# Performance work log

Measured on AMD Instinct MI355X. Metric: run time of the kernel, lower is better.

The kernel has to match this reference:

```python
import jax, jax.numpy as jnp
import numpy as np

BLOCK_SIZE = 32
EPS = 1e-6


def setup_inputs() -> dict:
    key = jax.random.key(0)
    k1, k2, k3, k4, k5 = jax.random.split(key, 5)
    B, H, L, D = 2, 16, 4096, 128
    return {
        "query_states": jax.random.normal(k1, (B, H, L, D), dtype=jnp.float32),
        "key_states": jax.random.normal(k2, (B, H, L, D), dtype=jnp.float32),
        "value_states": jax.random.normal(k3, (B, H, L, D), dtype=jnp.float32),
        # learned params; init near torch defaults (ones/zeros) with small noise
        "phi_scale": 1.0 + 0.1 * jax.random.normal(k4, (H, 1, D), dtype=jnp.float32),
        "phi_bias": 0.1 * jax.random.normal(k5, (H, 1, D), dtype=jnp.float32),
    }


def _forward(query_states, key_states, value_states, phi_scale, phi_bias):
    B, H, L, D = query_states.shape
    bs = BLOCK_SIZE
    N = L // bs  # L chosen divisible by block_size (no padding path)

    def feature_map(x):  # x: (B,H,N,bs,D)
        # phi_scale (H,1,D) -> (H,1,1,D) broadcasts over (B,H,N,bs,D)
        y = jax.nn.elu(x * phi_scale[:, None] + phi_bias[:, None]) + 1.0
        return jnp.clip(y, 0.0, 10.0)

    q = query_states.reshape(B, H, N, bs, D)
    k = key_states.reshape(B, H, N, bs, D)
    v = value_states.reshape(B, H, N, bs, D)

    phi_q = feature_map(q)
    phi_k = feature_map(k)

    # move block axis to front for scan: (N,B,H,bs,D)
    pq = jnp.moveaxis(phi_q, 2, 0)
    pk = jnp.moveaxis(phi_k, 2, 0)
    vb = jnp.moveaxis(v, 2, 0)

    S0 = jnp.zeros((B, H, D, D), dtype=jnp.float32)
    Z0 = jnp.zeros((B, H, D), dtype=jnp.float32)

    def step(carry, inp):
        S, Z = carry
        pq_n, pk_n, v_n = inp  # each (B,H,bs,D)
        # block-causal, bidirectional within block: update state BEFORE output
        S = S + jnp.einsum('bhkd,bhke->bhde', pk_n, v_n)
        Z = Z + pk_n.sum(axis=-2)
        num = jnp.einsum('bhqd,bhde->bhqe', pq_n, S)
        den = jnp.maximum(jnp.einsum('bhqd,bhd->bhq', pq_n, Z), EPS)
        return (S, Z), num / den[..., None]

    _, out_blocks = jax.lax.scan(step, (S0, Z0), (pq, pk, vb))  # (N,B,H,bs,D)
    out = jnp.moveaxis(out_blocks, 0, 2).reshape(B, H, L, D)
    return out


def reference(query_states, key_states, value_states, phi_scale, phi_bias):
    return _forward(query_states, key_states, value_states, phi_scale, phi_bias)
```

## Files before the change

kernel.cpp:

```cpp
#include <hip/hip_runtime.h>
#include <stdint.h>

#define BH 32
#define LSEQ 4096
#define DDIM 128
#define CHUNKS 16
#define CHUNK_ROWS 256
#define STATE_SZ (DDIM*DDIM + DDIM)

typedef __attribute__((ext_vector_type(8))) short bf16x8;
typedef __attribute__((ext_vector_type(4))) float f32x4;

__device__ inline uint16_t f2bf(float f) {
    uint32_t x = __builtin_bit_cast(uint32_t, f);
    x += 0x7fffu + ((x >> 16) & 1u);
    return (uint16_t)(x >> 16);
}
__device__ inline uint32_t pack2(float a, float b) {
    return (uint32_t)f2bf(a) | ((uint32_t)f2bf(b) << 16);
}
__device__ inline float phi_f(float x, float s, float b) {
    float y = fmaf(x, s, b);
    float pos = fminf(y + 1.0f, 10.0f);
    float neg = __expf(y);
    return (y > 0.0f) ? pos : neg;
}
__device__ inline void bar_lgkm() {
    asm volatile("s_waitcnt lgkmcnt(0)\n\ts_barrier" ::: "memory");
}

#define SMEM1 67584
__global__ __launch_bounds__(512, 2) void la_state(
    const float* __restrict__ K, const float* __restrict__ V,
    const float* __restrict__ scale, const float* __restrict__ bias,
    float* __restrict__ states)
{
    extern __shared__ char smem[];
    const int tid  = threadIdx.x;
    const int bh   = blockIdx.x >> 4;
    const int ch   = blockIdx.x & 15;
    const int h    = bh & 15;
    const int lane = tid & 63;
    const int wid  = tid >> 6;
    const int i15  = lane & 15;
    const int q4   = lane >> 4;
    const size_t base = (size_t)bh * LSEQ * DDIM;
    const int row0 = ch * CHUNK_ROWS;

    const int d  = tid & 127;
    const int rg = tid >> 7;
    const float sk = scale[h*DDIM + d];
    const float bk = bias [h*DDIM + d];

    f32x4 accS[8];
    #pragma unroll
    for (int mt = 0; mt < 8; ++mt) accS[mt] = (f32x4){0.f,0.f,0.f,0.f};
    float zacc = 0.f;

    float kreg[16], vreg[16];
    auto load_kv = [&](int g) {
        const float* Kc = K + base + (size_t)(row0 + 64*g + 16*rg)*DDIM + d;
        const float* Vc = V + base + (size_t)(row0 + 64*g + 16*rg)*DDIM + d;
        #pragma unroll
        for (int j = 0; j < 16; ++j) {
            kreg[j] = Kc[(size_t)j*DDIM];
            vreg[j] = Vc[(size_t)j*DDIM];
        }
    };
    auto stage = [&](int b) {
        uint32_t wk[8], wv8[8];
        #pragma unroll
        for (int j = 0; j < 8; ++j) {
            float p0 = phi_f(kreg[2*j],   sk, bk);
            float p1 = phi_f(kreg[2*j+1], sk, bk);
            zacc += p0 + p1;
            wk[j]  = pack2(p0, p1);
            wv8[j] = pack2(vreg[2*j], vreg[2*j+1]);
        }
        char* pkb = smem + b*16384;
        char* vtb = smem + 32768 + b*16384;
        const uint32_t lin = (uint32_t)(d*128 + 32*rg);
        const uint32_t swz = (uint32_t)((d & 7) << 4);
        *(uint4*)(pkb + ((lin     ) ^ swz)) = ((const uint4*)wk)[0];
        *(uint4*)(pkb + ((lin + 16) ^ swz)) = ((const uint4*)wk)[1];
        *(uint4*)(vtb + ((lin     ) ^ swz)) = ((const uint4*)wv8)[0];
        *(uint4*)(vtb + ((lin + 16) ^ swz)) = ((const uint4*)wv8)[1];
    };

    load_kv(0);
    stage(0);
    load_kv(1);
    bar_lgkm();

    #pragma unroll
    for (int g = 0; g < 4; ++g) {
        if (g < 3) stage((g+1)&1);
        if (g < 2) load_kv(g+2);
        const char* pkb = smem + (g&1)*16384;
        const char* vtb = smem + 32768 + (g&1)*16384;
        const uint32_t swz = (uint32_t)((i15 & 7) << 4);
        #pragma unroll
        for (int ksl = 0; ksl < 2; ++ksl) {
            bf16x8 bv = *(const bf16x8*)(vtb + (((uint32_t)((16*wid+i15)*128 + 64*ksl + 16*q4)) ^ swz));
            #pragma unroll
            for (int mt = 0; mt < 8; ++mt) {
                bf16x8 av = *(const bf16x8*)(pkb + (((uint32_t)((16*mt+i15)*128 + 64*ksl + 16*q4)) ^ swz));
                accS[mt] = __builtin_amdgcn_mfma_f32_16x16x32_bf16(av, bv, accS[mt], 0, 0, 0);
            }
        }
        bar_lgkm();
    }

    float* Zpart = (float*)(smem + 65536);
    Zpart[rg*128 + d] = zacc;
    float* stb = states + (size_t)(bh*CHUNKS + ch)*STATE_SZ;
    #pragma unroll
    for (int mt = 0; mt < 8; ++mt)
        #pragma unroll
        for (int r = 0; r < 4; ++r)
            stb[(size_t)(16*mt + 4*q4 + r)*DDIM + 16*wid + i15] = accS[mt][r];
    bar_lgkm();
    if (tid < 128)
        stb[DDIM*DDIM + tid] = Zpart[tid] + Zpart[128+tid] + Zpart[256+tid] + Zpart[384+tid];
}

__global__ void la_prefix(float* __restrict__ states) {
    const int bh  = blockIdx.y;
    const int idx = blockIdx.x * 128 + threadIdx.x;
    float* p = states + (size_t)bh * CHUNKS * STATE_SZ + idx;
    float run = 0.f;
    #pragma unroll
    for (int c = 0; c < CHUNKS; ++c) {
        float v = p[(size_t)c * STATE_SZ];
        p[(size_t)c * STATE_SZ] = run;
        run += v;
    }
}

#define SMEM2 71680
__global__ __launch_bounds__(512, 2) void la_fwd(
    const float* __restrict__ Q, const float* __restrict__ K,
    const float* __restrict__ V, const float* __restrict__ scale,
    const float* __restrict__ bias, const float* __restrict__ states,
    float* __restrict__ out)
{
    extern __shared__ char smem[];
    char* S0T  = smem;
    char* pkB  = smem + 32768;
    char* vtB  = smem + 49152;
    float* sbL  = (float*)(smem + 69632);
    float* denl = (float*)(smem + 70656);

    const int tid  = threadIdx.x;
    const int bh   = blockIdx.x >> 4;
    const int ch   = blockIdx.x & 15;
    const int h    = bh & 15;
    const int lane = tid & 63;
    const int wid  = tid >> 6;
    const int i15  = lane & 15;
    const int q4   = lane >> 4;
    const size_t base = (size_t)bh * LSEQ * DDIM;
    const int row0 = ch * CHUNK_ROWS;
    const float* stb = states + (size_t)(bh*CHUNKS + ch)*STATE_SZ;

    const int krow = tid >> 4;
    const int kc8  = (tid & 15) * 8;
    const int ve   = tid & 127;
    const int vrg  = tid >> 7;

    const int qa0 = wid, qa1 = 15 - wid;
    const int jmax0 = qa0 >> 1, jmax1 = qa1 >> 1;

    float4 kq[2];
    float  vr[8];
    auto load_kv = [&](int g) {
        const float* Kr = K + base + (size_t)(row0 + 32*g + krow)*DDIM + kc8;
        kq[0] = *(const float4*)(Kr);
        kq[1] = *(const float4*)(Kr + 4);
        const float* Vc = V + base + (size_t)(row0 + 32*g + 8*vrg)*DDIM + ve;
        #pragma unroll
        for (int j = 0; j < 8; ++j) vr[j] = Vc[(size_t)j*DDIM];
    };
    auto stage_kv = [&](int b) {
        float4 s0 = *(const float4*)&sbL[kc8];
        float4 s1 = *(const float4*)&sbL[kc8 + 4];
        float4 b0 = *(const float4*)&sbL[128 + kc8];
        float4 b1 = *(const float4*)&sbL[128 + kc8 + 4];
        uint32_t wk[4];
        wk[0] = pack2(phi_f(kq[0].x, s0.x, b0.x), phi_f(kq[0].y, s0.y, b0.y));
        wk[1] = pack2(phi_f(kq[0].z, s0.z, b0.z), phi_f(kq[0].w, s0.w, b0.w));
        wk[2] = pack2(phi_f(kq[1].x, s1.x, b1.x), phi_f(kq[1].y, s1.y, b1.y));
        wk[3] = pack2(phi_f(kq[1].z, s1.z, b1.z), phi_f(kq[1].w, s1.w, b1.w));
        const uint32_t lin = (uint32_t)(krow*256 + kc8*2);
        const uint32_t swz = (uint32_t)((krow & 7) << 4);
        *(uint4*)(pkB + b*8192 + (lin ^ swz)) = *(const uint4*)wk;
        uint32_t wv8[4];
        #pragma unroll
        for (int j = 0; j < 4; ++j) wv8[j] = pack2(vr[2*j], vr[2*j+1]);
        *(uint4*)(vtB + b*10240 + (uint32_t)(ve*80 + vrg*16)) = *(const uint4*)wv8;
    };

    load_kv(0);

    if (tid < 256) sbL[tid] = (tid < 128) ? scale[h*DDIM + tid] : bias[h*DDIM + tid - 128];

    {
        const int se  = tid & 127;
        const int sdg = tid >> 7;
        const uint32_t swz = (uint32_t)((se & 7) << 4);
        #pragma unroll
        for (int pass = 0; pass < 2; ++pass) {
            float sv[16];
            const float* sp = stb + (size_t)(32*sdg + 16*pass)*DDIM + se;
            #pragma unroll
            for (int k2 = 0; k2 < 16; ++k2) sv[k2] = sp[(size_t)k2*DDIM];
            uint32_t wbuf[8];
            #pragma unroll
            for (int k2 = 0; k2 < 8; ++k2) wbuf[k2] = pack2(sv[2*k2], sv[2*k2+1]);
            const uint32_t linb = (uint32_t)(se*256 + (32*sdg + 16*pass)*2);
            *(uint4*)(S0T + ((linb     ) ^ swz)) = ((const uint4*)wbuf)[0];
            *(uint4*)(S0T + ((linb + 16) ^ swz)) = ((const uint4*)wbuf)[1];
        }
    }

    bf16x8 pq[2][4];
    float dden0 = 0.f, dden1 = 0.f;
    #pragma unroll
    for (int ks = 0; ks < 4; ++ks) {
        const float* sp = scale + h*DDIM + 32*ks + 8*q4;
        const float* bp = bias  + h*DDIM + 32*ks + 8*q4;
        const float* zp = stb + DDIM*DDIM + 32*ks + 8*q4;
        float4 s0 = *(const float4*)sp, s1 = *(const float4*)(sp+4);
        float4 b0 = *(const float4*)bp, b1 = *(const float4*)(bp+4);
        float4 z0 = *(const float4*)zp, z1 = *(const float4*)(zp+4);
        #pragma unroll
        for (int tl = 0; tl < 2; ++tl) {
            const int a = tl ? qa1 : qa0;
            const float* qp = Q + base + (size_t)(row0 + 16*a + i15)*DDIM + 32*ks + 8*q4;
            float4 a0 = *(const float4*)qp, a1 = *(const float4*)(qp+4);
            float f0 = phi_f(a0.x, s0.x, b0.x), f1 = phi_f(a0.y, s0.y, b0.y);
            float f2 = phi_f(a0.z, s0.z, b0.z), f3 = phi_f(a0.w, s0.w, b0.w);
            float f4 = phi_f(a1.x, s1.x, b1.x), f5 = phi_f(a1.y, s1.y, b1.y);
            float f6 = phi_f(a1.z, s1.z, b1.z), f7 = phi_f(a1.w, s1.w, b1.w);
            float ds = f0*z0.x + f1*z0.y + f2*z0.z + f3*z0.w
                     + f4*z1.x + f5*z1.y + f6*z1.z + f7*z1.w;
            if (tl == 0) dden0 += ds; else dden1 += ds;
            uint4 uu = { pack2(f0,f1), pack2(f2,f3), pack2(f4,f5), pack2(f6,f7) };
            pq[tl][ks] = __builtin_bit_cast(bf16x8, uu);
        }
    }

    stage_kv(0);
    load_kv(1);
    bar_lgkm();

    f32x4 acc[2][8];
    #pragma unroll
    for (int tl = 0; tl < 2; ++tl)
        #pragma unroll
        for (int et = 0; et < 8; ++et) acc[tl][et] = (f32x4){0.f,0.f,0.f,0.f};
    {
        const uint32_t swz = (uint32_t)((i15 & 7) << 4);
        #pragma unroll
        for (int ks = 0; ks < 4; ++ks)
            #pragma unroll
            for (int et = 0; et < 8; ++et) {
                bf16x8 sb = *(const bf16x8*)(S0T + (((uint32_t)((16*et+i15)*256 + (32*ks + 8*q4)*2)) ^ swz));
                acc[0][et] = __builtin_amdgcn_mfma_f32_16x16x32_bf16(pq[0][ks], sb, acc[0][et], 0, 0, 0);
                acc[1][et] = __builtin_amdgcn_mfma_f32_16x16x32_bf16(pq[1][ks], sb, acc[1][et], 0, 0, 0);
            }
    }
    stage_kv(1);
    load_kv(2);
    bar_lgkm();

    char* Ascr0 = S0T + wid*2560;
    char* Ascr1 = Ascr0 + 1280;
    const uint32_t swzf = (uint32_t)((i15 & 7) << 4);

    #pragma unroll
    for (int t = 0; t < 8; ++t) {
        if (t >= 1) {
            if (t + 1 <= 7) stage_kv((t+1)&1);
            if (t + 2 <= 7) load_kv(t+2);
        }
        const char* pk = pkB + (t&1)*8192;
        const char* vt = vtB + (t&1)*10240;
        #pragma unroll
        for (int tl = 0; tl < 2; ++tl) {
            const int jm = tl ? jmax1 : jmax0;
            if (t <= jm) {
                char* As = tl ? Ascr1 : Ascr0;
                f32x4 Aacc[2];
                Aacc[0] = (f32x4){0.f,0.f,0.f,0.f};
                Aacc[1] = (f32x4){0.f,0.f,0.f,0.f};
                #pragma unroll
                for (int ks = 0; ks < 4; ++ks) {
                    bf16x8 ak0 = *(const bf16x8*)(pk + (((uint32_t)((     i15)*256 + (32*ks + 8*q4)*2)) ^ swzf));
                    bf16x8 ak1 = *(const bf16x8*)(pk + (((uint32_t)((16 + i15)*256 + (32*ks + 8*q4)*2)) ^ swzf));
                    bf16x8 pqv = tl ? pq[1][ks] : pq[0][ks];
                    Aacc[0] = __builtin_amdgcn_mfma_f32_16x16x32_bf16(ak0, pqv, Aacc[0], 0, 0, 0);
                    Aacc[1] = __builtin_amdgcn_mfma_f32_16x16x32_bf16(ak1, pqv, Aacc[1], 0, 0, 0);
                }
                float dsum = Aacc[0][0]+Aacc[0][1]+Aacc[0][2]+Aacc[0][3]
                           + Aacc[1][0]+Aacc[1][1]+Aacc[1][2]+Aacc[1][3];
                if (tl == 0) dden0 += dsum; else dden1 += dsum;
                #pragma unroll
                for (int sub = 0; sub < 2; ++sub) {
                    uint2 o;
                    o.x = pack2(Aacc[sub][0], Aacc[sub][1]);
                    o.y = pack2(Aacc[sub][2], Aacc[sub][3]);
                    *(uint2*)(As + (uint32_t)((i15*40 + 16*sub + 4*q4)*2)) = o;
                }
                bf16x8 aq = *(const bf16x8*)(As + (uint32_t)((i15*40 + 8*q4)*2));
                #pragma unroll
                for (int et = 0; et < 8; ++et) {
                    bf16x8 bv = *(const bf16x8*)(vt + (uint32_t)((16*et+i15)*80 + q4*16));
                    acc[tl][et] = __builtin_amdgcn_mfma_f32_16x16x32_bf16(aq, bv, acc[tl][et], 0, 0, 0);
                }
            }
        }
        bar_lgkm();
    }

    dden0 += __shfl_xor(dden0, 16, 64); dden0 += __shfl_xor(dden0, 32, 64);
    dden1 += __shfl_xor(dden1, 16, 64); dden1 += __shfl_xor(dden1, 32, 64);
    if (q4 == 0) {
        denl[wid*32 + i15]      = dden0;
        denl[wid*32 + 16 + i15] = dden1;
    }
    #pragma unroll
    for (int tl = 0; tl < 2; ++tl) {
        const int a = tl ? qa1 : qa0;
        float inv[4];
        #pragma unroll
        for (int r = 0; r < 4; ++r)
            inv[r] = 1.0f / fmaxf(denl[wid*32 + 16*tl + 4*q4 + r], 1e-6f);
        #pragma unroll
        for (int et = 0; et < 8; ++et)
            #pragma unroll
            for (int r = 0; r < 4; ++r)
                out[base + (size_t)(row0 + 16*a + 4*q4 + r)*DDIM + 16*et + i15] =
                    acc[tl][et][r] * inv[r];
    }
}

extern "C" void kernel_launch(void* const* d_in, const int* in_sizes, int n_in,
                              void* d_out, int out_size, void* d_ws, size_t ws_size,
                              hipStream_t stream) {
    const float* Q     = (const float*)d_in[0];
    const float* K     = (const float*)d_in[1];
    const float* V     = (const float*)d_in[2];
    const float* scale = (const float*)d_in[3];
    const float* bias  = (const float*)d_in[4];
    float* out    = (float*)d_out;
    float* states = (float*)d_ws;

    static bool s_attr = false;
    if (!s_attr) {
        hipFuncSetAttribute(reinterpret_cast<const void*>(la_state),
                            hipFuncAttributeMaxDynamicSharedMemorySize, SMEM1);
        hipFuncSetAttribute(reinterpret_cast<const void*>(la_fwd),
                            hipFuncAttributeMaxDynamicSharedMemorySize, SMEM2);
        s_attr = true;
    }

    hipLaunchKernelGGL(la_state, dim3(BH*CHUNKS), dim3(512), SMEM1, stream,
                       K, V, scale, bias, states);
    hipLaunchKernelGGL(la_prefix, dim3(129, BH), dim3(128), 0, stream, states);
    hipLaunchKernelGGL(la_fwd, dim3(BH*CHUNKS), dim3(512), SMEM2, stream,
                       Q, K, V, scale, bias, states, out);
}
```

Before: 284.8 us.

## Split each chunk's query rows across two blocks with XCD-aware block remapping

The forward kernel now launches twice as many blocks. Each block handles 128 query rows, half of a 256-row chunk, with one 16-row tile per wave instead of two balanced tiles. Blocks are remapped so the two halves and neighbouring chunks land on the same XCD, and the second half iterates over all 8 key groups while the first half iterates over 4. This is meant to raise parallelism and occupancy and to reduce register pressure. In exchange, the S0 state is reloaded and converted twice per chunk, and the two halves carry unequal work, which costs the load balance the old paired tiles gave.

```diff
diff --git a/kernel.cpp b/kernel.cpp
--- a/kernel.cpp
+++ b/kernel.cpp
@@ -137,7 +137,7 @@
     }
 }
 
-#define SMEM2 71680
+#define SMEM2 71168
 __global__ __launch_bounds__(512, 2) void la_fwd(
     const float* __restrict__ Q, const float* __restrict__ K,
     const float* __restrict__ V, const float* __restrict__ scale,
@@ -152,24 +152,28 @@
     float* denl = (float*)(smem + 70656);
 
     const int tid  = threadIdx.x;
-    const int bh   = blockIdx.x >> 4;
-    const int ch   = blockIdx.x & 15;
+    const int b    = blockIdx.x;
+    const int lid  = ((b & 7) << 7) | (b >> 3);
+    const int half = lid & 1;
+    const int cgid = lid >> 1;
+    const int bh   = cgid >> 4;
+    const int ch   = cgid & 15;
     const int h    = bh & 15;
     const int lane = tid & 63;
     const int wid  = tid >> 6;
     const int i15  = lane & 15;
     const int q4   = lane >> 4;
     const size_t base = (size_t)bh * LSEQ * DDIM;
-    const int row0 = ch * CHUNK_ROWS;
+    const int row0  = ch * CHUNK_ROWS;
+    const int qrow0 = row0 + half*128;
+    const int NG    = 4 + 4*half;
+    const int jm    = 4*half + (wid >> 1);
     const float* stb = states + (size_t)(bh*CHUNKS + ch)*STATE_SZ;
 
     const int krow = tid >> 4;
     const int kc8  = (tid & 15) * 8;
     const int ve   = tid & 127;
     const int vrg  = tid >> 7;
-
-    const int qa0 = wid, qa1 = 15 - wid;
-    const int jmax0 = qa0 >> 1, jmax1 = qa1 >> 1;
 
     float4 kq[2];
     float  vr[8];
@@ -181,7 +185,7 @@
         #pragma unroll
         for (int j = 0; j < 8; ++j) vr[j] = Vc[(size_t)j*DDIM];
     };
-    auto stage_kv = [&](int b) {
+    auto stage_kv = [&](int bb) {
         float4 s0 = *(const float4*)&sbL[kc8];
         float4 s1 = *(const float4*)&sbL[kc8 + 4];
         float4 b0 = *(const float4*)&sbL[128 + kc8];
@@ -193,11 +197,11 @@
         wk[3] = pack2(phi_f(kq[1].z, s1.z, b1.z), phi_f(kq[1].w, s1.w, b1.w));
         const uint32_t lin = (uint32_t)(krow*256 + kc8*2);
         const uint32_t swz = (uint32_t)((krow & 7) << 4);
-        *(uint4*)(pkB + b*8192 + (lin ^ swz)) = *(const uint4*)wk;
+        *(uint4*)(pkB + bb*8192 + (lin ^ swz)) = *(const uint4*)wk;
         uint32_t wv8[4];
         #pragma unroll
         for (int j = 0; j < 4; ++j) wv8[j] = pack2(vr[2*j], vr[2*j+1]);
-        *(uint4*)(vtB + b*10240 + (uint32_t)(ve*80 + vrg*16)) = *(const uint4*)wv8;
+        *(uint4*)(vtB + bb*10240 + (uint32_t)(ve*80 + vrg*16)) = *(const uint4*)wv8;
     };
 
     load_kv(0);
@@ -223,8 +227,8 @@
         }
     }
 
-    bf16x8 pq[2][4];
-    float dden0 = 0.f, dden1 = 0.f;
+    bf16x8 pq[4];
+    float dden = 0.f;
     #pragma unroll
     for (int ks = 0; ks < 4; ++ks) {
         const float* sp = scale + h*DDIM + 32*ks + 8*q4;
@@ -233,32 +237,25 @@
         float4 s0 = *(const float4*)sp, s1 = *(const float4*)(sp+4);
         float4 b0 = *(const float4*)bp, b1 = *(const float4*)(bp+4);
         float4 z0 = *(const float4*)zp, z1 = *(const float4*)(zp+4);
-        #pragma unroll
-        for (int tl = 0; tl < 2; ++tl) {
-            const int a = tl ? qa1 : qa0;
-            const float* qp = Q + base + (size_t)(row0 + 16*a + i15)*DDIM + 32*ks + 8*q4;
-            float4 a0 = *(const float4*)qp, a1 = *(const float4*)(qp+4);
-            float f0 = phi_f(a0.x, s0.x, b0.x), f1 = phi_f(a0.y, s0.y, b0.y);
-            float f2 = phi_f(a0.z, s0.z, b0.z), f3 = phi_f(a0.w, s0.w, b0.w);
-            float f4 = phi_f(a1.x, s1.x, b1.x), f5 = phi_f(a1.y, s1.y, b1.y);
-            float f6 = phi_f(a1.z, s1.z, b1.z), f7 = phi_f(a1.w, s1.w, b1.w);
-            float ds = f0*z0.x + f1*z0.y + f2*z0.z + f3*z0.w
-                     + f4*z1.x + f5*z1.y + f6*z1.z + f7*z1.w;
-            if (tl == 0) dden0 += ds; else dden1 += ds;
-            uint4 uu = { pack2(f0,f1), pack2(f2,f3), pack2(f4,f5), pack2(f6,f7) };
-            pq[tl][ks] = __builtin_bit_cast(bf16x8, uu);
-        }
+        const float* qp = Q + base + (size_t)(qrow0 + 16*wid + i15)*DDIM + 32*ks + 8*q4;
+        float4 a0 = *(const float4*)qp, a1 = *(const float4*)(qp+4);
+        float f0 = phi_f(a0.x, s0.x, b0.x), f1 = phi_f(a0.y, s0.y, b0.y);
+        float f2 = phi_f(a0.z, s0.z, b0.z), f3 = phi_f(a0.w, s0.w, b0.w);
+        float f4 = phi_f(a1.x, s1.x, b1.x), f5 = phi_f(a1.y, s1.y, b1.y);
+        float f6 = phi_f(a1.z, s1.z, b1.z), f7 = phi_f(a1.w, s1.w, b1.w);
+        dden += f0*z0.x + f1*z0.y + f2*z0.z + f3*z0.w
+              + f4*z1.x + f5*z1.y + f6*z1.z + f7*z1.w;
+        uint4 uu = { pack2(f0,f1), pack2(f2,f3), pack2(f4,f5), pack2(f6,f7) };
+        pq[ks] = __builtin_bit_cast(bf16x8, uu);
     }
 
     stage_kv(0);
     load_kv(1);
     bar_lgkm();
 
-    f32x4 acc[2][8];
-    #pragma unroll
-    for (int tl = 0; tl < 2; ++tl)
-        #pragma unroll
-        for (int et = 0; et < 8; ++et) acc[tl][et] = (f32x4){0.f,0.f,0.f,0.f};
+    f32x4 acc[8];
+    #pragma unroll
+    for (int et = 0; et < 8; ++et) acc[et] = (f32x4){0.f,0.f,0.f,0.f};
     {
         const uint32_t swz = (uint32_t)((i15 & 7) << 4);
         #pragma unroll
@@ -266,83 +263,66 @@
             #pragma unroll
             for (int et = 0; et < 8; ++et) {
                 bf16x8 sb = *(const bf16x8*)(S0T + (((uint32_t)((16*et+i15)*256 + (32*ks + 8*q4)*2)) ^ swz));
-                acc[0][et] = __builtin_amdgcn_mfma_f32_16x16x32_bf16(pq[0][ks], sb, acc[0][et], 0, 0, 0);
-                acc[1][et] = __builtin_amdgcn_mfma_f32_16x16x32_bf16(pq[1][ks], sb, acc[1][et], 0, 0, 0);
+                acc[et] = __builtin_amdgcn_mfma_f32_16x16x32_bf16(pq[ks], sb, acc[et], 0, 0, 0);
             }
     }
     stage_kv(1);
-    load_kv(2);
+    if (NG > 2) load_kv(2);
     bar_lgkm();
 
-    char* Ascr0 = S0T + wid*2560;
-    char* Ascr1 = Ascr0 + 1280;
+    char* Ascr = S0T + wid*1280;
     const uint32_t swzf = (uint32_t)((i15 & 7) << 4);
 
-    #pragma unroll
-    for (int t = 0; t < 8; ++t) {
+    for (int t = 0; t < NG; ++t) {
         if (t >= 1) {
-            if (t + 1 <= 7) stage_kv((t+1)&1);
-            if (t + 2 <= 7) load_kv(t+2);
+            if (t + 1 < NG) stage_kv((t+1)&1);
+            if (t + 2 < NG) load_kv(t+2);
         }
         const char* pk = pkB + (t&1)*8192;
         const char* vt = vtB + (t&1)*10240;
-        #pragma unroll
-        for (int tl = 0; tl < 2; ++tl) {
-            const int jm = tl ? jmax1 : jmax0;
-            if (t <= jm) {
-                char* As = tl ? Ascr1 : Ascr0;
-                f32x4 Aacc[2];
-                Aacc[0] = (f32x4){0.f,0.f,0.f,0.f};
-                Aacc[1] = (f32x4){0.f,0.f,0.f,0.f};
-                #pragma unroll
-                for (int ks = 0; ks < 4; ++ks) {
-                    bf16x8 ak0 = *(const bf16x8*)(pk + (((uint32_t)((     i15)*256 + (32*ks + 8*q4)*2)) ^ swzf));
-                    bf16x8 ak1 = *(const bf16x8*)(pk + (((uint32_t)((16 + i15)*256 + (32*ks + 8*q4)*2)) ^ swzf));
-                    bf16x8 pqv = tl ? pq[1][ks] : pq[0][ks];
-                    Aacc[0] = __builtin_amdgcn_mfma_f32_16x16x32_bf16(ak0, pqv, Aacc[0], 0, 0, 0);
-                    Aacc[1] = __builtin_amdgcn_mfma_f32_16x16x32_bf16(ak1, pqv, Aacc[1], 0, 0, 0);
-                }
-                float dsum = Aacc[0][0]+Aacc[0][1]+Aacc[0][2]+Aacc[0][3]
-                           + Aacc[1][0]+Aacc[1][1]+Aacc[1][2]+Aacc[1][3];
-                if (tl == 0) dden0 += dsum; else dden1 += dsum;
-                #pragma unroll
-                for (int sub = 0; sub < 2; ++sub) {
-                    uint2 o;
-                    o.x = pack2(Aacc[sub][0], Aacc[sub][1]);
-                    o.y = pack2(Aacc[sub][2], Aacc[sub][3]);
-                    *(uint2*)(As + (uint32_t)((i15*40 + 16*sub + 4*q4)*2)) = o;
-                }
-                bf16x8 aq = *(const bf16x8*)(As + (uint32_t)((i15*40 + 8*q4)*2));
-                #pragma unroll
-                for (int et = 0; et < 8; ++et) {
-                    bf16x8 bv = *(const bf16x8*)(vt + (uint32_t)((16*et+i15)*80 + q4*16));
-                    acc[tl][et] = __builtin_amdgcn_mfma_f32_16x16x32_bf16(aq, bv, acc[tl][et], 0, 0, 0);
-                }
+        if (t <= jm) {
+            f32x4 Aacc[2];
+            Aacc[0] = (f32x4){0.f,0.f,0.f,0.f};
+            Aacc[1] = (f32x4){0.f,0.f,0.f,0.f};
+            #pragma unroll
+            for (int ks = 0; ks < 4; ++ks) {
+                bf16x8 ak0 = *(const bf16x8*)(pk + (((uint32_t)((     i15)*256 + (32*ks + 8*q4)*2)) ^ swzf));
+                bf16x8 ak1 = *(const bf16x8*)(pk + (((uint32_t)((16 + i15)*256 + (32*ks + 8*q4)*2)) ^ swzf));
+                Aacc[0] = __builtin_amdgcn_mfma_f32_16x16x32_bf16(ak0, pq[ks], Aacc[0], 0, 0, 0);
+                Aacc[1] = __builtin_amdgcn_mfma_f32_16x16x32_bf16(ak1, pq[ks], Aacc[1], 0, 0, 0);
+            }
+            dden += Aacc[0][0]+Aacc[0][1]+Aacc[0][2]+Aacc[0][3]
+                  + Aacc[1][0]+Aacc[1][1]+Aacc[1][2]+Aacc[1][3];
+            #pragma unroll
+            for (int sub = 0; sub < 2; ++sub) {
+                uint2 o;
+                o.x = pack2(Aacc[sub][0], Aacc[sub][1]);
+                o.y = pack2(Aacc[sub][2], Aacc[sub][3]);
+                *(uint2*)(Ascr + (uint32_t)((i15*40 + 16*sub + 4*q4)*2)) = o;
+            }
+            bf16x8 aq = *(const bf16x8*)(Ascr + (uint32_t)((i15*40 + 8*q4)*2));
+            #pragma unroll
+            for (int et = 0; et < 8; ++et) {
+                bf16x8 bv = *(const bf16x8*)(vt + (uint32_t)((16*et+i15)*80 + q4*16));
+                acc[et] = __builtin_amdgcn_mfma_f32_16x16x32_bf16(aq, bv, acc[et], 0, 0, 0);
             }
         }
         bar_lgkm();
     }
 
-    dden0 += __shfl_xor(dden0, 16, 64); dden0 += __shfl_xor(dden0, 32, 64);
-    dden1 += __shfl_xor(dden1, 16, 64); dden1 += __shfl_xor(dden1, 32, 64);
-    if (q4 == 0) {
-        denl[wid*32 + i15]      = dden0;
-        denl[wid*32 + 16 + i15] = dden1;
-    }
-    #pragma unroll
-    for (int tl = 0; tl < 2; ++tl) {
-        const int a = tl ? qa1 : qa0;
-        float inv[4];
+    dden += __shfl_xor(dden, 16, 64);
+    dden += __shfl_xor(dden, 32, 64);
+    if (q4 == 0) denl[wid*16 + i15] = dden;
+    float inv[4];
+    #pragma unroll
+    for (int r = 0; r < 4; ++r)
+        inv[r] = 1.0f / fmaxf(denl[wid*16 + 4*q4 + r], 1e-6f);
+    #pragma unroll
+    for (int et = 0; et < 8; ++et)
         #pragma unroll
         for (int r = 0; r < 4; ++r)
-            inv[r] = 1.0f / fmaxf(denl[wid*32 + 16*tl + 4*q4 + r], 1e-6f);
-        #pragma unroll
-        for (int et = 0; et < 8; ++et)
-            #pragma unroll
-            for (int r = 0; r < 4; ++r)
-                out[base + (size_t)(row0 + 16*a + 4*q4 + r)*DDIM + 16*et + i15] =
-                    acc[tl][et][r] * inv[r];
-    }
+            out[base + (size_t)(qrow0 + 16*wid + 4*q4 + r)*DDIM + 16*et + i15] =
+                acc[et][r] * inv[r];
 }
 
 extern "C" void kernel_launch(void* const* d_in, const int* in_sizes, int n_in,
@@ -368,6 +348,6 @@
     hipLaunchKernelGGL(la_state, dim3(BH*CHUNKS), dim3(512), SMEM1, stream,
                        K, V, scale, bias, states);
     hipLaunchKernelGGL(la_prefix, dim3(129, BH), dim3(128), 0, stream, states);
-    hipLaunchKernelGGL(la_fwd, dim3(BH*CHUNKS), dim3(512), SMEM2, stream,
+    hipLaunchKernelGGL(la_fwd, dim3(BH*CHUNKS*2), dim3(512), SMEM2, stream,
                        Q, K, V, scale, bias, states, out);
 }
```

After: 290.9 us. 2.2% more time.

## Shrink LDS footprints, stream S0 in quarters, vectorize prefix scan

Applied to the files above, without the earlier changes.

la_state now stages 32-row groups instead of 64, which halves its LDS buffers and raises the launch bound to three blocks per CU. la_fwd loads the carried state S0 in four 32-column quarters that are double-buffered and interleaved with K/V staging and the inter-chunk MFMAs, which cuts LDS from about 70KB to 54KB. la_prefix now works on float4 with a quarter of the blocks, and the max-dynamic-shared-memory attribute calls are removed. The costs are more barriers and loop iterations. Dropping the attribute calls is only safe if both new sizes stay under the default LDS limit.

```diff
diff --git a/kernel.cpp b/kernel.cpp
--- a/kernel.cpp
+++ b/kernel.cpp
@@ -29,8 +29,8 @@
     asm volatile("s_waitcnt lgkmcnt(0)\n\ts_barrier" ::: "memory");
 }
 
-#define SMEM1 67584
-__global__ __launch_bounds__(512, 2) void la_state(
+#define SMEM1 34816
+__global__ __launch_bounds__(512, 3) void la_state(
     const float* __restrict__ K, const float* __restrict__ V,
     const float* __restrict__ scale, const float* __restrict__ bias,
     float* __restrict__ states)
@@ -57,34 +57,29 @@
     for (int mt = 0; mt < 8; ++mt) accS[mt] = (f32x4){0.f,0.f,0.f,0.f};
     float zacc = 0.f;
 
-    float kreg[16], vreg[16];
+    float kreg[8], vreg[8];
     auto load_kv = [&](int g) {
-        const float* Kc = K + base + (size_t)(row0 + 64*g + 16*rg)*DDIM + d;
-        const float* Vc = V + base + (size_t)(row0 + 64*g + 16*rg)*DDIM + d;
-        #pragma unroll
-        for (int j = 0; j < 16; ++j) {
+        const float* Kc = K + base + (size_t)(row0 + 32*g + 8*rg)*DDIM + d;
+        const float* Vc = V + base + (size_t)(row0 + 32*g + 8*rg)*DDIM + d;
+        #pragma unroll
+        for (int j = 0; j < 8; ++j) {
             kreg[j] = Kc[(size_t)j*DDIM];
             vreg[j] = Vc[(size_t)j*DDIM];
         }
     };
     auto stage = [&](int b) {
-        uint32_t wk[8], wv8[8];
-        #pragma unroll
-        for (int j = 0; j < 8; ++j) {
+        uint32_t wk[4], wv[4];
+        #pragma unroll
+        for (int j = 0; j < 4; ++j) {
             float p0 = phi_f(kreg[2*j],   sk, bk);
             float p1 = phi_f(kreg[2*j+1], sk, bk);
             zacc += p0 + p1;
-            wk[j]  = pack2(p0, p1);
-            wv8[j] = pack2(vreg[2*j], vreg[2*j+1]);
-        }
-        char* pkb = smem + b*16384;
-        char* vtb = smem + 32768 + b*16384;
-        const uint32_t lin = (uint32_t)(d*128 + 32*rg);
-        const uint32_t swz = (uint32_t)((d & 7) << 4);
-        *(uint4*)(pkb + ((lin     ) ^ swz)) = ((const uint4*)wk)[0];
-        *(uint4*)(pkb + ((lin + 16) ^ swz)) = ((const uint4*)wk)[1];
-        *(uint4*)(vtb + ((lin     ) ^ swz)) = ((const uint4*)wv8)[0];
-        *(uint4*)(vtb + ((lin + 16) ^ swz)) = ((const uint4*)wv8)[1];
+            wk[j] = pack2(p0, p1);
+            wv[j] = pack2(vreg[2*j], vreg[2*j+1]);
+        }
+        const uint32_t off = ((uint32_t)(d*64 + rg*16)) ^ ((uint32_t)((d&7)<<4));
+        *(uint4*)(smem + b*8192 + off)         = *(const uint4*)wk;
+        *(uint4*)(smem + 16384 + b*8192 + off) = *(const uint4*)wv;
     };
 
     load_kv(0);
@@ -92,26 +87,22 @@
     load_kv(1);
     bar_lgkm();
 
-    #pragma unroll
-    for (int g = 0; g < 4; ++g) {
-        if (g < 3) stage((g+1)&1);
-        if (g < 2) load_kv(g+2);
-        const char* pkb = smem + (g&1)*16384;
-        const char* vtb = smem + 32768 + (g&1)*16384;
-        const uint32_t swz = (uint32_t)((i15 & 7) << 4);
-        #pragma unroll
-        for (int ksl = 0; ksl < 2; ++ksl) {
-            bf16x8 bv = *(const bf16x8*)(vtb + (((uint32_t)((16*wid+i15)*128 + 64*ksl + 16*q4)) ^ swz));
-            #pragma unroll
-            for (int mt = 0; mt < 8; ++mt) {
-                bf16x8 av = *(const bf16x8*)(pkb + (((uint32_t)((16*mt+i15)*128 + 64*ksl + 16*q4)) ^ swz));
-                accS[mt] = __builtin_amdgcn_mfma_f32_16x16x32_bf16(av, bv, accS[mt], 0, 0, 0);
-            }
+    for (int g = 0; g < 8; ++g) {
+        if (g + 1 < 8) stage((g+1)&1);
+        if (g + 2 < 8) load_kv(g+2);
+        const char* pkb = smem + (g&1)*8192;
+        const char* vtb = smem + 16384 + (g&1)*8192;
+        const uint32_t swz = (uint32_t)((i15&7)<<4);
+        bf16x8 bv = *(const bf16x8*)(vtb + (((uint32_t)((16*wid+i15)*64 + q4*16)) ^ swz));
+        #pragma unroll
+        for (int mt = 0; mt < 8; ++mt) {
+            bf16x8 av = *(const bf16x8*)(pkb + (((uint32_t)((16*mt+i15)*64 + q4*16)) ^ swz));
+            accS[mt] = __builtin_amdgcn_mfma_f32_16x16x32_bf16(av, bv, accS[mt], 0, 0, 0);
         }
         bar_lgkm();
     }
 
-    float* Zpart = (float*)(smem + 65536);
+    float* Zpart = (float*)(smem + 32768);
     Zpart[rg*128 + d] = zacc;
     float* stb = states + (size_t)(bh*CHUNKS + ch)*STATE_SZ;
     #pragma unroll
@@ -127,17 +118,18 @@
 __global__ void la_prefix(float* __restrict__ states) {
     const int bh  = blockIdx.y;
     const int idx = blockIdx.x * 128 + threadIdx.x;
-    float* p = states + (size_t)bh * CHUNKS * STATE_SZ + idx;
-    float run = 0.f;
+    if (idx >= STATE_SZ/4) return;
+    float4* p = (float4*)(states + (size_t)bh * CHUNKS * STATE_SZ) + idx;
+    float4 run = {0.f, 0.f, 0.f, 0.f};
     #pragma unroll
     for (int c = 0; c < CHUNKS; ++c) {
-        float v = p[(size_t)c * STATE_SZ];
-        p[(size_t)c * STATE_SZ] = run;
-        run += v;
-    }
-}
-
-#define SMEM2 71680
+        float4 v = p[(size_t)c * (STATE_SZ/4)];
+        p[(size_t)c * (STATE_SZ/4)] = run;
+        run.x += v.x; run.y += v.y; run.z += v.z; run.w += v.w;
+    }
+}
+
+#define SMEM2 55296
 __global__ __launch_bounds__(512, 2) void la_fwd(
     const float* __restrict__ Q, const float* __restrict__ K,
     const float* __restrict__ V, const float* __restrict__ scale,
@@ -145,11 +137,11 @@
     float* __restrict__ out)
 {
     extern __shared__ char smem[];
-    char* S0T  = smem;
-    char* pkB  = smem + 32768;
-    char* vtB  = smem + 49152;
-    float* sbL  = (float*)(smem + 69632);
-    float* denl = (float*)(smem + 70656);
+    char* S0q  = smem;
+    char* pkB  = smem + 16384;
+    char* vtB  = smem + 32768;
+    float* sbL  = (float*)(smem + 53248);
+    float* denl = (float*)(smem + 54272);
 
     const int tid  = threadIdx.x;
     const int bh   = blockIdx.x >> 4;
@@ -167,9 +159,11 @@
     const int kc8  = (tid & 15) * 8;
     const int ve   = tid & 127;
     const int vrg  = tid >> 7;
+    const int se32  = tid & 31;
+    const int sdg32 = tid >> 5;
 
     const int qa0 = wid, qa1 = 15 - wid;
-    const int jmax0 = qa0 >> 1, jmax1 = qa1 >> 1;
+    const int jm0 = qa0 >> 1, jm1 = qa1 >> 1;
 
     float4 kq[2];
     float  vr[8];
@@ -181,7 +175,7 @@
         #pragma unroll
         for (int j = 0; j < 8; ++j) vr[j] = Vc[(size_t)j*DDIM];
     };
-    auto stage_kv = [&](int b) {
+    auto stage_kv = [&](int bb) {
         float4 s0 = *(const float4*)&sbL[kc8];
         float4 s1 = *(const float4*)&sbL[kc8 + 4];
         float4 b0 = *(const float4*)&sbL[128 + kc8];
@@ -193,35 +187,31 @@
         wk[3] = pack2(phi_f(kq[1].z, s1.z, b1.z), phi_f(kq[1].w, s1.w, b1.w));
         const uint32_t lin = (uint32_t)(krow*256 + kc8*2);
         const uint32_t swz = (uint32_t)((krow & 7) << 4);
-        *(uint4*)(pkB + b*8192 + (lin ^ swz)) = *(const uint4*)wk;
-        uint32_t wv8[4];
-        #pragma unroll
-        for (int j = 0; j < 4; ++j) wv8[j] = pack2(vr[2*j], vr[2*j+1]);
-        *(uint4*)(vtB + b*10240 + (uint32_t)(ve*80 + vrg*16)) = *(const uint4*)wv8;
+        *(uint4*)(pkB + bb*8192 + (lin ^ swz)) = *(const uint4*)wk;
+        uint32_t wv[4];
+        #pragma unroll
+        for (int j = 0; j < 4; ++j) wv[j] = pack2(vr[2*j], vr[2*j+1]);
+        *(uint4*)(vtB + bb*10240 + (uint32_t)(ve*80 + vrg*16)) = *(const uint4*)wv;
+    };
+
+    float sv[8];
+    auto s0_load = [&](int qt) {
+        const float* sp = stb + (size_t)(8*sdg32)*DDIM + 32*qt + se32;
+        #pragma unroll
+        for (int j = 0; j < 8; ++j) sv[j] = sp[(size_t)j*DDIM];
+    };
+    auto s0_write = [&](int qt) {
+        uint32_t w[4];
+        #pragma unroll
+        for (int j = 0; j < 4; ++j) w[j] = pack2(sv[2*j], sv[2*j+1]);
+        const uint32_t lin = (uint32_t)(se32*256 + sdg32*16);
+        const uint32_t swz = (uint32_t)((se32 & 7) << 4);
+        *(uint4*)(S0q + (qt&1)*8192 + (lin ^ swz)) = *(const uint4*)w;
     };
 
     load_kv(0);
-
     if (tid < 256) sbL[tid] = (tid < 128) ? scale[h*DDIM + tid] : bias[h*DDIM + tid - 128];
-
-    {
-        const int se  = tid & 127;
-        const int sdg = tid >> 7;
-        const uint32_t swz = (uint32_t)((se & 7) << 4);
-        #pragma unroll
-        for (int pass = 0; pass < 2; ++pass) {
-            float sv[16];
-            const float* sp = stb + (size_t)(32*sdg + 16*pass)*DDIM + se;
-            #pragma unroll
-            for (int k2 = 0; k2 < 16; ++k2) sv[k2] = sp[(size_t)k2*DDIM];
-            uint32_t wbuf[8];
-            #pragma unroll
-            for (int k2 = 0; k2 < 8; ++k2) wbuf[k2] = pack2(sv[2*k2], sv[2*k2+1]);
-            const uint32_t linb = (uint32_t)(se*256 + (32*sdg + 16*pass)*2);
-            *(uint4*)(S0T + ((linb     ) ^ swz)) = ((const uint4*)wbuf)[0];
-            *(uint4*)(S0T + ((linb + 16) ^ swz)) = ((const uint4*)wbuf)[1];
-        }
-    }
+    s0_load(0);
 
     bf16x8 pq[2][4];
     float dden0 = 0.f, dden1 = 0.f;
@@ -249,9 +239,7 @@
             pq[tl][ks] = __builtin_bit_cast(bf16x8, uu);
         }
     }
-
-    stage_kv(0);
-    load_kv(1);
+    s0_write(0);
     bar_lgkm();
 
     f32x4 acc[2][8];
@@ -259,26 +247,43 @@
     for (int tl = 0; tl < 2; ++tl)
         #pragma unroll
         for (int et = 0; et < 8; ++et) acc[tl][et] = (f32x4){0.f,0.f,0.f,0.f};
-    {
+
+    auto term1q = [&](int qt, int qb) {
         const uint32_t swz = (uint32_t)((i15 & 7) << 4);
         #pragma unroll
         for (int ks = 0; ks < 4; ++ks)
             #pragma unroll
-            for (int et = 0; et < 8; ++et) {
-                bf16x8 sb = *(const bf16x8*)(S0T + (((uint32_t)((16*et+i15)*256 + (32*ks + 8*q4)*2)) ^ swz));
+            for (int etl = 0; etl < 2; ++etl) {
+                const int et = 2*qt + etl;
+                bf16x8 sb = *(const bf16x8*)(S0q + qb*8192 +
+                    (((uint32_t)((16*etl+i15)*256 + (32*ks + 8*q4)*2)) ^ swz));
                 acc[0][et] = __builtin_amdgcn_mfma_f32_16x16x32_bf16(pq[0][ks], sb, acc[0][et], 0, 0, 0);
                 acc[1][et] = __builtin_amdgcn_mfma_f32_16x16x32_bf16(pq[1][ks], sb, acc[1][et], 0, 0, 0);
             }
-    }
+    };
+
+    s0_load(1);
+    stage_kv(0);
+    load_kv(1);
+    term1q(0, 0);
+    s0_write(1);
+    bar_lgkm();
+    s0_load(2);
     stage_kv(1);
     load_kv(2);
-    bar_lgkm();
-
-    char* Ascr0 = S0T + wid*2560;
-    char* Ascr1 = Ascr0 + 1280;
+    term1q(1, 1);
+    s0_write(2);
+    bar_lgkm();
+    s0_load(3);
+    term1q(2, 0);
+    s0_write(3);
+    bar_lgkm();
+    term1q(3, 1);
+    bar_lgkm();
+
+    char* Ascr = smem + wid*1280;
     const uint32_t swzf = (uint32_t)((i15 & 7) << 4);
 
-    #pragma unroll
     for (int t = 0; t < 8; ++t) {
         if (t >= 1) {
             if (t + 1 <= 7) stage_kv((t+1)&1);
@@ -288,9 +293,8 @@
         const char* vt = vtB + (t&1)*10240;
         #pragma unroll
         for (int tl = 0; tl < 2; ++tl) {
-            const int jm = tl ? jmax1 : jmax0;
+            const int jm = tl ? jm1 : jm0;
             if (t <= jm) {
-                char* As = tl ? Ascr1 : Ascr0;
                 f32x4 Aacc[2];
                 Aacc[0] = (f32x4){0.f,0.f,0.f,0.f};
                 Aacc[1] = (f32x4){0.f,0.f,0.f,0.f};
@@ -310,9 +314,9 @@
                     uint2 o;
                     o.x = pack2(Aacc[sub][0], Aacc[sub][1]);
                     o.y = pack2(Aacc[sub][2], Aacc[sub][3]);
-                    *(uint2*)(As + (uint32_t)((i15*40 + 16*sub + 4*q4)*2)) = o;
+                    *(uint2*)(Ascr + (uint32_t)((i15*40 + 16*sub + 4*q4)*2)) = o;
                 }
-                bf16x8 aq = *(const bf16x8*)(As + (uint32_t)((i15*40 + 8*q4)*2));
+                bf16x8 aq = *(const bf16x8*)(Ascr + (uint32_t)((i15*40 + 8*q4)*2));
                 #pragma unroll
                 for (int et = 0; et < 8; ++et) {
                     bf16x8 bv = *(const bf16x8*)(vt + (uint32_t)((16*et+i15)*80 + q4*16));
@@ -356,18 +360,9 @@
     float* out    = (float*)d_out;
     float* states = (float*)d_ws;
 
-    static bool s_attr = false;
-    if (!s_attr) {
-        hipFuncSetAttribute(reinterpret_cast<const void*>(la_state),
-                            hipFuncAttributeMaxDynamicSharedMemorySize, SMEM1);
-        hipFuncSetAttribute(reinterpret_cast<const void*>(la_fwd),
-                            hipFuncAttributeMaxDynamicSharedMemorySize, SMEM2);
-        s_attr = true;
-    }
-
     hipLaunchKernelGGL(la_state, dim3(BH*CHUNKS), dim3(512), SMEM1, stream,
                        K, V, scale, bias, states);
-    hipLaunchKernelGGL(la_prefix, dim3(129, BH), dim3(128), 0, stream, states);
+    hipLaunchKernelGGL(la_prefix, dim3(33, BH), dim3(128), 0, stream, states);
     hipLaunchKernelGGL(la_fwd, dim3(BH*CHUNKS), dim3(512), SMEM2, stream,
                        Q, K, V, scale, bias, states, out);
 }
```

Result: faster. 278.7 us (-2.1%).
